# Optimization experiments

Measured on AMD Instinct MI355X. Metric: run time of the kernel, lower is better.

## Reference

```python
import jax, jax.numpy as jnp
import numpy as np

D = 4096
B = 2
S = 2048


def setup_inputs() -> dict:
    key = jax.random.key(0)
    k1, k2, k3, k4 = jax.random.split(key, 4)
    x = jax.random.normal(k1, (B, S, D), dtype=jnp.float32)
    # 2-bit symmetric quantized codes stored as uint8 in torch; torch's
    # clamp(-1,1).to(uint8) wraps -1 -> 255, so codes span {0,1,255}-like
    # values. We draw the full uint8 range for a representative baseline.
    q_int = jax.random.randint(k2, (D, D), 0, 256, dtype=jnp.int32)
    # per-channel positive scales (small, like 2-bit scales: |w|max / 1)
    scale = jax.random.uniform(k3, (D,), dtype=jnp.float32) * 0.01 + 1e-4
    # symmetric quantization -> zero_point = 0 per channel (int buffer)
    zero_point = jnp.zeros((D,), dtype=jnp.int32)
    bias = jax.random.normal(k4, (D,), dtype=jnp.float32) * 0.02
    return {"x": x, "q_int": q_int, "scale": scale,
            "zero_point": zero_point, "bias": bias}


def reference(x, q_int, scale, zero_point, bias):
    # Faithful to FFQLinear.forward:
    #   weight = (q_int.float() - zero_point) * scale
    # NOTE: no unsqueeze(-1) here (unlike pack time), so scale/zp broadcast
    # over the LAST (column) axis of the [d, d] code matrix.
    zp = zero_point.astype(jnp.float32)
    W = (q_int.astype(jnp.float32) - zp[None, :]) * scale[None, :]  # [D, D]
    b, s, d = x.shape
    # F.linear(x2d, W.t(), bias) == x2d @ W + bias
    out = jnp.einsum('bsd,dk->bsk', x, W) + bias  # [B, S, D]
    return out
```

## Files before the change

### kernel.cpp

```cpp
#include <hip/hip_runtime.h>
#include <stdint.h>

typedef unsigned short u16;
typedef __attribute__((ext_vector_type(8))) short short8;
typedef __attribute__((ext_vector_type(4))) float f32x4;

#define KD 4096

typedef const __attribute__((address_space(1))) void* gas1_t;
typedef __attribute__((address_space(3))) void* las3_t;

__device__ __forceinline__ void g2l16(const void* g, void* l) {
  __builtin_amdgcn_global_load_lds((gas1_t)g, (las3_t)l, 16, 0, 0);
}

__device__ __forceinline__ u16 f2bf(float f) {
  uint32_t u = __float_as_uint(f);
  return (u16)((u + 0x7FFFu + ((u >> 16) & 1u)) >> 16);
}

__global__ __launch_bounds__(256)
void cvt_fused(const float4* __restrict__ x, const int* __restrict__ q,
               const int* __restrict__ zp, uint2* __restrict__ xb,
               u16* __restrict__ qt) {
  const int b = blockIdx.x;
  if (b >= 4096) {
    int gid = (b - 4096) * 256 + threadIdx.x;
    float4 f = x[gid];
    union { u16 u[4]; uint2 v; } o;
    o.u[0] = f2bf(f.x); o.u[1] = f2bf(f.y);
    o.u[2] = f2bf(f.z); o.u[3] = f2bf(f.w);
    xb[gid] = o.v;
    return;
  }
  __shared__ uint32_t P[32][68];
  const int n0 = (b & 63) * 64;
  const int k0 = (b >> 6) * 64;
  const int nc = threadIdx.x & 15;
  const int kr = threadIdx.x >> 4;

  int z[4];
#pragma unroll
  for (int j = 0; j < 4; ++j) z[j] = zp[n0 + nc * 4 + j];

#pragma unroll
  for (int s = 0; s < 2; ++s) {
    const int kp = kr + s * 16;
    const int64_t rb = (int64_t)(k0 + kp * 2) * KD + n0 + nc * 4;
    int4 r0 = *(const int4*)(q + rb);
    int4 r1 = *(const int4*)(q + rb + KD);
    uint4 w;
    w.x = (uint32_t)f2bf((float)(r0.x - z[0])) | ((uint32_t)f2bf((float)(r1.x - z[0])) << 16);
    w.y = (uint32_t)f2bf((float)(r0.y - z[1])) | ((uint32_t)f2bf((float)(r1.y - z[1])) << 16);
    w.z = (uint32_t)f2bf((float)(r0.z - z[2])) | ((uint32_t)f2bf((float)(r1.z - z[2])) << 16);
    w.w = (uint32_t)f2bf((float)(r0.w - z[3])) | ((uint32_t)f2bf((float)(r1.w - z[3])) << 16);
    *(uint4*)&P[kp][nc * 4] = w;
  }
  __syncthreads();

  const int kq = threadIdx.x & 7;
  const int nn = threadIdx.x >> 3;
#pragma unroll
  for (int p = 0; p < 2; ++p) {
    const int n = nn + p * 32;
    uint4 v;
    v.x = P[kq * 4 + 0][n];
    v.y = P[kq * 4 + 1][n];
    v.z = P[kq * 4 + 2][n];
    v.w = P[kq * 4 + 3][n];
    *(uint4*)(qt + (int64_t)(n0 + n) * KD + k0 + kq * 8) = v;
  }
}

__global__ __launch_bounds__(512, 2)
void gemm8(const u16* __restrict__ A, const u16* __restrict__ Bt,
           const float* __restrict__ scale, const float* __restrict__ bias,
           float* __restrict__ C) {
  __shared__ u16 lds[65536];

  const int tid = threadIdx.x;
  const int orig = blockIdx.x;
  const int lid = (orig & 7) * 32 + (orig >> 3);
  const int bm0 = (lid >> 4) * 256;
  const int bn0 = (lid & 15) * 256;

  const int lane = tid & 63;
  const int w = tid >> 6;
  const int wr = w >> 2;
  const int wc = w & 3;
  const int l15 = lane & 15;
  const int q4 = lane >> 4;
  const int l7 = l15 & 7;

  const int rl = tid >> 3;
  const int csw = (tid & 7) ^ (rl & 7);
  const u16* gA = A + (int64_t)(bm0 + rl) * KD + csw * 8;
  const u16* gB = Bt + (int64_t)(bn0 + rl) * KD + csw * 8;

#define STA(OFF, qq, kt) g2l16(gA + (int64_t)(qq) * 64 * KD + (kt), &lds[(OFF) + (qq) * 4096 + tid * 8])
#define STB(OFF, qq, kt) g2l16(gB + (int64_t)(qq) * 64 * KD + (kt), &lds[(OFF) + (qq) * 4096 + tid * 8])

#define RD_A(AOFF, mh)                                                        \
  do {                                                                        \
    _Pragma("unroll") for (int m = 0; m < 4; ++m) {                           \
      const int row = wr * 128 + (mh) * 64 + m * 16 + l15;                    \
      _Pragma("unroll") for (int kk = 0; kk < 2; ++kk)                        \
        ar[m][kk] = *(const short8*)&lds[(AOFF) + row * 64 + (((kk * 4 + q4) ^ l7) * 8)]; \
    }                                                                         \
  } while (0)

#define RD_B(BOFF, nn0)                                                       \
  do {                                                                        \
    _Pragma("unroll") for (int n = 0; n < 2; ++n) {                           \
      const int col = wc * 64 + ((nn0) + n) * 16 + l15;                       \
      _Pragma("unroll") for (int kk = 0; kk < 2; ++kk)                        \
        br[(nn0) + n][kk] = *(const short8*)&lds[(BOFF) + col * 64 + (((kk * 4 + q4) ^ l7) * 8)]; \
    }                                                                         \
  } while (0)

#define MFMA_Q(mb, nn0)                                                       \
  do {                                                                        \
    __builtin_amdgcn_s_setprio(1);                                            \
    _Pragma("unroll") for (int m = 0; m < 4; ++m)                             \
      _Pragma("unroll") for (int n = 0; n < 2; ++n)                           \
        _Pragma("unroll") for (int kk = 0; kk < 2; ++kk)                      \
          acc[(mb) + m][(nn0) + n] = __builtin_amdgcn_mfma_f32_16x16x32_bf16( \
              ar[m][kk], br[(nn0) + n][kk], acc[(mb) + m][(nn0) + n], 0, 0, 0); \
    __builtin_amdgcn_s_setprio(0);                                            \
  } while (0)

#define BAR __builtin_amdgcn_s_barrier()
#define SCHED0 __builtin_amdgcn_sched_barrier(0)
#define LGKM0 do { asm volatile("s_waitcnt lgkmcnt(0)" ::: "memory"); SCHED0; } while (0)
#define LGKM8 asm volatile("s_waitcnt lgkmcnt(8)" ::: "memory")
#define VMC6 asm volatile("s_waitcnt vmcnt(6)" ::: "memory")
#define VMC2 asm volatile("s_waitcnt vmcnt(2)" ::: "memory")
#define VMC0 asm volatile("s_waitcnt vmcnt(0)" ::: "memory")
#define WNONE

#define K_TILE(AOFF, BOFF, SAOFF, SBOFF, KTN, STG, W1, W2)                    \
  do {                                                                        \
                                                                     \
    RD_A(AOFF, 0);                                                            \
    RD_B(BOFF, 0);                                                            \
    if (STG) { STB(SBOFF, 0, KTN); STB(SBOFF, 1, KTN); STA(SAOFF, 0, KTN); }  \
    LGKM8;                                                                    \
    BAR; LGKM0;                                                               \
    MFMA_Q(0, 0);                                                             \
    BAR;                                                                      \
                                                                     \
    RD_B(BOFF, 2);                                                            \
    if (STG) { STB(SBOFF, 2, KTN); STB(SBOFF, 3, KTN); STA(SAOFF, 2, KTN); }  \
    W1;                                                                       \
    BAR; LGKM0;                                                               \
    MFMA_Q(0, 2);                                                             \
    BAR;                                                                      \
                                                                     \
    RD_A(AOFF, 1);                                                            \
    if (STG) { STA(SAOFF, 1, KTN); STA(SAOFF, 3, KTN); }                      \
    BAR; LGKM0;                                                               \
    MFMA_Q(4, 0);                                                             \
    BAR;                                                                      \
                                                                     \
    W2;                                                                       \
    BAR; LGKM0;                                                               \
    MFMA_Q(4, 2);                                                             \
    BAR;                                                                      \
  } while (0)

  f32x4 acc[8][4];
#pragma unroll
  for (int m = 0; m < 8; ++m)
#pragma unroll
    for (int n = 0; n < 4; ++n) acc[m][n] = (f32x4)(0.f);

  short8 ar[4][2], br[4][2];

  STB(16384, 0, 0); STB(16384, 1, 0); STA(0, 0, 0);
  STB(16384, 2, 0); STB(16384, 3, 0); STA(0, 2, 0);
  STA(0, 1, 0); STA(0, 3, 0);
  VMC2;
  BAR;

  for (int i = 0; i < 31; ++i) {
    const int kt1 = (2 * i + 1) * 64;
    const int kt2 = (2 * i + 2) * 64;
    K_TILE(0, 16384, 32768, 49152, kt1, 1, VMC6, VMC2);
    K_TILE(32768, 49152, 0, 16384, kt2, 1, VMC6, VMC2);
  }
  K_TILE(0, 16384, 32768, 49152, 63 * 64, 1, VMC6, VMC2);
  K_TILE(32768, 49152, 0, 16384, 0, 0, VMC0, WNONE);

  const int r4 = q4 * 4;
#pragma unroll
  for (int n = 0; n < 4; ++n) {
    const int col = bn0 + wc * 64 + n * 16 + l15;
    const float sc = scale[col];
    const float bs = bias[col];
#pragma unroll
    for (int mi = 0; mi < 8; ++mi) {
      const int row = bm0 + wr * 128 + mi * 16 + r4;
#pragma unroll
      for (int j = 0; j < 4; ++j)
        C[(int64_t)(row + j) * KD + col] = acc[mi][n][j] * sc + bs;
    }
  }
}

extern "C" void kernel_launch(void* const* d_in, const int* in_sizes, int n_in,
                              void* d_out, int out_size, void* d_ws, size_t ws_size,
                              hipStream_t stream) {
  const float* x = (const float*)d_in[0];
  const int* q = (const int*)d_in[1];
  const float* scale = (const float*)d_in[2];
  const int* zp = (const int*)d_in[3];
  const float* bias = (const float*)d_in[4];
  float* out = (float*)d_out;

  u16* Xb = (u16*)d_ws;
  u16* Qt = Xb + (size_t)4096 * 4096;

  cvt_fused<<<20480, 256, 0, stream>>>((const float4*)x, q, zp,
                                       (uint2*)Xb, Qt);

  gemm8<<<256, 512, 0, stream>>>(Xb, Qt, scale, bias, out);
}
```

Before: 279.2 us.

## Reorder B-tile LDS layout and staging so first MFMA quarter waits on less data

New measurement: 276.0 us. About the same (-1.2%).

```diff
diff --git a/kernel.cpp b/kernel.cpp
--- a/kernel.cpp
+++ b/kernel.cpp
@@ -95,10 +95,16 @@
   const int rl = tid >> 3;
   const int csw = (tid & 7) ^ (rl & 7);
   const u16* gA = A + (int64_t)(bm0 + rl) * KD + csw * 8;
-  const u16* gB = Bt + (int64_t)(bn0 + rl) * KD + csw * 8;
+  const int rr = (rl & 31) + ((rl >> 5) << 6);
+  const u16* gBe = Bt + (int64_t)(bn0 + rr) * KD + csw * 8;
+  const u16* gBo = gBe + (int64_t)32 * KD;
+
+  const int bq = (wc & 1) * 32 + l15;
+  const int bub = wc >> 1;
 
 #define STA(OFF, qq, kt) g2l16(gA + (int64_t)(qq) * 64 * KD + (kt), &lds[(OFF) + (qq) * 4096 + tid * 8])
-#define STB(OFF, qq, kt) g2l16(gB + (int64_t)(qq) * 64 * KD + (kt), &lds[(OFF) + (qq) * 4096 + tid * 8])
+#define STBE(OFF, uu, kt) g2l16(gBe + (int64_t)(uu) * 128 * KD + (kt), &lds[(OFF) + (uu) * 4096 + tid * 8])
+#define STBO(OFF, uu, kt) g2l16(gBo + (int64_t)(uu) * 128 * KD + (kt), &lds[(OFF) + (2 + (uu)) * 4096 + tid * 8])
 
 #define RD_A(AOFF, mh)                                                        \
   do {                                                                        \
@@ -112,9 +118,9 @@
 #define RD_B(BOFF, nn0)                                                       \
   do {                                                                        \
     _Pragma("unroll") for (int n = 0; n < 2; ++n) {                           \
-      const int col = wc * 64 + ((nn0) + n) * 16 + l15;                       \
+      const int ro = ((nn0) + bub) * 4096 + (bq + n * 16) * 64;               \
       _Pragma("unroll") for (int kk = 0; kk < 2; ++kk)                        \
-        br[(nn0) + n][kk] = *(const short8*)&lds[(BOFF) + col * 64 + (((kk * 4 + q4) ^ l7) * 8)]; \
+        br[(nn0) + n][kk] = *(const short8*)&lds[(BOFF) + ro + (((kk * 4 + q4) ^ l7) * 8)]; \
     }                                                                         \
   } while (0)
 
@@ -134,23 +140,26 @@
 #define LGKM0 do { asm volatile("s_waitcnt lgkmcnt(0)" ::: "memory"); SCHED0; } while (0)
 #define LGKM8 asm volatile("s_waitcnt lgkmcnt(8)" ::: "memory")
 #define VMC6 asm volatile("s_waitcnt vmcnt(6)" ::: "memory")
+#define VMC4 asm volatile("s_waitcnt vmcnt(4)" ::: "memory")
 #define VMC2 asm volatile("s_waitcnt vmcnt(2)" ::: "memory")
 #define VMC0 asm volatile("s_waitcnt vmcnt(0)" ::: "memory")
 #define WNONE
 
-#define K_TILE(AOFF, BOFF, SAOFF, SBOFF, KTN, STG, W1, W2)                    \
+#define K_TILE(AOFF, BOFF, SAOFF, SBOFF, KTN, STG, W0, W1, W2)                \
   do {                                                                        \
                                                                      \
     RD_A(AOFF, 0);                                                            \
     RD_B(BOFF, 0);                                                            \
-    if (STG) { STB(SBOFF, 0, KTN); STB(SBOFF, 1, KTN); STA(SAOFF, 0, KTN); }  \
+    if (STG) { STBE(SBOFF, 0, KTN); STBE(SBOFF, 1, KTN);                      \
+               STA(SAOFF, 0, KTN); STA(SAOFF, 2, KTN); }                      \
+    W0;                                                                       \
     LGKM8;                                                                    \
     BAR; LGKM0;                                                               \
     MFMA_Q(0, 0);                                                             \
     BAR;                                                                      \
                                                                      \
     RD_B(BOFF, 2);                                                            \
-    if (STG) { STB(SBOFF, 2, KTN); STB(SBOFF, 3, KTN); STA(SAOFF, 2, KTN); }  \
+    if (STG) { STBO(SBOFF, 0, KTN); STBO(SBOFF, 1, KTN); }                    \
     W1;                                                                       \
     BAR; LGKM0;                                                               \
     MFMA_Q(0, 2);                                                             \
@@ -176,20 +185,18 @@
 
   short8 ar[4][2], br[4][2];
 
-  STB(16384, 0, 0); STB(16384, 1, 0); STA(0, 0, 0);
-  STB(16384, 2, 0); STB(16384, 3, 0); STA(0, 2, 0);
+  STBE(16384, 0, 0); STBE(16384, 1, 0); STA(0, 0, 0); STA(0, 2, 0);
+  STBO(16384, 0, 0); STBO(16384, 1, 0);
   STA(0, 1, 0); STA(0, 3, 0);
-  VMC2;
+  VMC4;
   BAR;
 
   for (int i = 0; i < 31; ++i) {
-    const int kt1 = (2 * i + 1) * 64;
-    const int kt2 = (2 * i + 2) * 64;
-    K_TILE(0, 16384, 32768, 49152, kt1, 1, VMC6, VMC2);
-    K_TILE(32768, 49152, 0, 16384, kt2, 1, VMC6, VMC2);
-  }
-  K_TILE(0, 16384, 32768, 49152, 63 * 64, 1, VMC6, VMC2);
-  K_TILE(32768, 49152, 0, 16384, 0, 0, VMC0, WNONE);
+    K_TILE(0, 16384, 32768, 49152, (2 * i + 1) * 64, 1, VMC6, VMC6, VMC4);
+    K_TILE(32768, 49152, 0, 16384, (2 * i + 2) * 64, 1, VMC6, VMC6, VMC4);
+  }
+  K_TILE(0, 16384, 32768, 49152, 63 * 64, 1, VMC6, VMC6, VMC4);
+  K_TILE(32768, 49152, 0, 16384, 0, 0, VMC2, VMC0, WNONE);
 
   const int r4 = q4 * 4;
 #pragma unroll
```
